# Performance work log

Hardware: AMD Instinct MI355X
Metric: run time of the kernel (lower is better)

Reference implementation:

```python
import jax, jax.numpy as jnp
import numpy as np

B, S, E, H = 4, 2048, 1024, 16
D = E // H  # head_dim = 64

def setup_inputs() -> dict:
    key = jax.random.key(0)
    ks = jax.random.split(key, 9)
    std = 1.0 / np.sqrt(E)
    return {
        "x":  jax.random.normal(ks[0], (B, S, E), jnp.float32),
        "Wq": jax.random.uniform(ks[1], (E, E), jnp.float32, -std, std),
        "bq": jax.random.uniform(ks[2], (E,),   jnp.float32, -std, std),
        "Wk": jax.random.uniform(ks[3], (E, E), jnp.float32, -std, std),
        "bk": jax.random.uniform(ks[4], (E,),   jnp.float32, -std, std),
        "Wv": jax.random.uniform(ks[5], (E, E), jnp.float32, -std, std),
        "bv": jax.random.uniform(ks[6], (E,),   jnp.float32, -std, std),
        "Wo": jax.random.uniform(ks[7], (E, E), jnp.float32, -std, std),
        "bo": jax.random.uniform(ks[8], (E,),   jnp.float32, -std, std),
    }

def reference(x, Wq, bq, Wk, bk, Wv, bv, Wo, bo):
    b, s, e = x.shape
    # QKV projections (weights stored as [in,out] == torch W.T applied as x @ W)
    q = (x @ Wq + bq).reshape(b, s, H, D).transpose(0, 2, 1, 3)  # [B,H,S,D]
    k = (x @ Wk + bk).reshape(b, s, H, D).transpose(0, 2, 1, 3)
    v = (x @ Wv + bv).reshape(b, s, H, D).transpose(0, 2, 1, 3)
    scores = jnp.einsum('bhqd,bhkd->bhqk', q, k) / jnp.sqrt(jnp.float32(D))
    causal = jnp.triu(jnp.ones((s, s), bool), k=1)  # True above diagonal
    scores = jnp.where(causal, -jnp.inf, scores)
    p = jax.nn.softmax(scores, axis=-1)  # dropout disabled (eval mode)
    out = jnp.einsum('bhqk,bhkd->bhqd', p, v)  # [B,H,S,D]
    out = out.transpose(0, 2, 1, 3).reshape(b, s, e)
    return out @ Wo + bo
```

## Files before the change

### kernel.cpp

```cpp
#include <hip/hip_runtime.h>
#include <math.h>

#define E_DIM 1024
#define B_DIM 4
#define S_DIM 2048
#define H_DIM 16
#define D_HEAD 64
#define M_DIM (B_DIM * S_DIM)
#define LOG2E 1.44269504f

typedef _Float16 half8 __attribute__((ext_vector_type(8)));
typedef _Float16 half4 __attribute__((ext_vector_type(4)));
typedef __fp16  fp16x2 __attribute__((ext_vector_type(2)));
typedef float floatx4 __attribute__((ext_vector_type(4)));
typedef unsigned uint2v __attribute__((ext_vector_type(2)));
#define MFMA_F16(a, b, c) __builtin_amdgcn_mfma_f32_16x16x32_f16(a, b, c, 0, 0, 0)

#if __has_builtin(__builtin_amdgcn_exp2f)
#define EXP2F(x) __builtin_amdgcn_exp2f(x)
#else
#define EXP2F(x) exp2f(x)
#endif

union H4 { fp16x2 h2[2]; half4 h4; };
union H8 { fp16x2 h2[4]; half8 h8; };

#define GLDS16(g, l)                                                          \
    __builtin_amdgcn_global_load_lds(                                         \
        (const __attribute__((address_space(1))) void*)(g),                   \
        (__attribute__((address_space(3))) void*)(l), 16, 0, 0)

__device__ const int QBAL[16] = {15,13,11,9, 0,2,4,6, 14,12,10,8, 1,3,5,7};

__global__ __launch_bounds__(256) void cvt_all(
    const float* __restrict__ X, _Float16* __restrict__ Xh,
    const float* __restrict__ W0, const float* __restrict__ W1,
    const float* __restrict__ W2, const float* __restrict__ W3,
    _Float16* __restrict__ T0, _Float16* __restrict__ T1,
    _Float16* __restrict__ T2, _Float16* __restrict__ T3)
{
    const int Lb = blockIdx.x;
    const int tid = threadIdx.x;
    if (Lb < 4096) {
        size_t i = ((size_t)Lb * 256 + tid) * 8;
        float4 a = *(const float4*)&X[i];
        float4 b = *(const float4*)&X[i + 4];
        half8 h = {(_Float16)a.x, (_Float16)a.y, (_Float16)a.z, (_Float16)a.w,
                   (_Float16)b.x, (_Float16)b.y, (_Float16)b.z, (_Float16)b.w};
        *(half8*)&Xh[i] = h;
        return;
    }
    const int L = Lb - 4096;
    const int z = L >> 8;
    const int rem = L & 255;
    const int k0 = (rem & 15) * 64, n0 = (rem >> 4) * 64;
    const float* W = (z == 0) ? W0 : (z == 1) ? W1 : (z == 2) ? W2 : W3;
    _Float16*   T  = (z == 0) ? T0 : (z == 1) ? T1 : (z == 2) ? T2 : T3;
    __shared__ float t[64][65];
#pragma unroll
    for (int it = 0; it < 4; it++) {
        int r = it * 16 + (tid >> 4);
        int c = (tid & 15) * 4;
        float4 v = *(const float4*)&W[(size_t)(k0 + r) * E_DIM + n0 + c];
        t[r][c] = v.x; t[r][c + 1] = v.y; t[r][c + 2] = v.z; t[r][c + 3] = v.w;
    }
    __syncthreads();
#pragma unroll
    for (int it = 0; it < 2; it++) {
        int n = it * 32 + (tid >> 3);
        int kk = (tid & 7) * 8;
        half8 h;
#pragma unroll
        for (int j = 0; j < 8; j++) h[j] = (_Float16)t[kk + j][n];
        *(half8*)&T[(size_t)(n0 + n) * E_DIM + k0 + kk] = h;
    }
}

#define STAGE128(t, s)                                                        \
    _Pragma("unroll") for (int i = 0; i < 4; i++) {                           \
        GLDS16(aS[i] + (t) * 64, As + (s) * 8192 + dOff[i]);                  \
        GLDS16(bS[i] + (t) * 64, Bs + (s) * 8192 + dOff[i]);                  \
    }

#define PH128_READ_A(mh)                                                      \
    _Pragma("unroll") for (int am = 0; am < 2; am++)                          \
        _Pragma("unroll") for (int kh = 0; kh < 2; kh++)                      \
            a_[am][kh] = *(const half8*)&As[sb +                              \
                (wr * 64 + ((mh) * 2 + am) * 16 + m16) * 64 +                 \
                (((kh * 4 + quad) ^ sw8) * 8)];

#define PH128_READ_B(nh)                                                      \
    _Pragma("unroll") for (int bn = 0; bn < 2; bn++)                          \
        _Pragma("unroll") for (int kh = 0; kh < 2; kh++)                      \
            b_[bn][kh] = *(const half8*)&Bs[sb +                              \
                (wc * 64 + ((nh) * 2 + bn) * 16 + m16) * 64 +                 \
                (((kh * 4 + quad) ^ sw8) * 8)];

#define PH128_MFMA(mh, nh)                                                    \
    __builtin_amdgcn_s_setprio(1);                                            \
    _Pragma("unroll") for (int am = 0; am < 2; am++)                          \
        _Pragma("unroll") for (int bn = 0; bn < 2; bn++)                      \
            acc[(mh) * 2 + am][(nh) * 2 + bn] =                               \
                MFMA_F16(a_[am][1], b_[bn][1],                                \
                    MFMA_F16(a_[am][0], b_[bn][0],                            \
                             acc[(mh) * 2 + am][(nh) * 2 + bn]));             \
    __builtin_amdgcn_s_setprio(0);

#define GEMM128_CORE(Aptr, Bptr)                                              \
    const int tid = threadIdx.x;                                              \
    const int wave = tid >> 6, lane = tid & 63;                               \
    const int m16 = lane & 15, quad = lane >> 4;                              \
    const int wr = wave >> 1, wc = wave & 1;                                  \
    const int m0 = blockIdx.x * 128, n0 = blockIdx.y * 128;                   \
    const int sw8 = m16 & 7;                                                  \
    __shared__ _Float16 As[2 * 8192];                                         \
    __shared__ _Float16 Bs[2 * 8192];                                         \
    floatx4 acc[4][4];                                                        \
    const floatx4 zf = {0.f, 0.f, 0.f, 0.f};                                  \
    _Pragma("unroll") for (int i = 0; i < 4; i++)                             \
        _Pragma("unroll") for (int j = 0; j < 4; j++) acc[i][j] = zf;         \
    const _Float16* aS[4];                                                    \
    const _Float16* bS[4];                                                    \
    int dOff[4];                                                              \
    _Pragma("unroll") for (int i = 0; i < 4; i++) {                           \
        int u = i * 256 + tid;                                                \
        int ru = u >> 3, cb = (u & 7) ^ (ru & 7);                             \
        aS[i] = (Aptr) + (size_t)(m0 + ru) * E_DIM + cb * 8;                  \
        bS[i] = (Bptr) + (size_t)(n0 + ru) * E_DIM + cb * 8;                  \
        dOff[i] = i * 2048 + wave * 512;                                      \
    }                                                                         \
    STAGE128(0, 0);                                                           \
    STAGE128(1, 1);                                                           \
    asm volatile("s_waitcnt vmcnt(8)" ::: "memory");                          \
    __builtin_amdgcn_s_barrier();                                             \
    half8 a_[2][2], b_[2][2];                                                 \
    for (int t = 0; t < 16; t++) {                                            \
        const int sb = (t & 1) * 8192;                                        \
        PH128_READ_A(0); PH128_READ_B(0); PH128_MFMA(0, 0);                   \
        PH128_READ_B(1); PH128_MFMA(0, 1);                                    \
        PH128_READ_A(1); PH128_MFMA(1, 1);                                    \
        PH128_READ_B(0); PH128_MFMA(1, 0);                                    \
        if (t + 1 < 16) {                                                     \
            asm volatile("s_waitcnt lgkmcnt(0)" ::: "memory");                \
            __builtin_amdgcn_s_barrier();                                     \
            if (t + 2 < 16) {                                                 \
                STAGE128(t + 2, t & 1);                                       \
                asm volatile("s_waitcnt vmcnt(8)" ::: "memory");              \
            } else {                                                          \
                asm volatile("s_waitcnt vmcnt(0)" ::: "memory");              \
            }                                                                 \
            __builtin_amdgcn_s_barrier();                                     \
        }                                                                     \
    }

__global__ __launch_bounds__(256) void qkv_mfma(
    const _Float16* __restrict__ Xh,
    const _Float16* __restrict__ Tq, const float* __restrict__ bq,
    const _Float16* __restrict__ Tk, const float* __restrict__ bk,
    const _Float16* __restrict__ Tv, const float* __restrict__ bv,
    _Float16* __restrict__ Qo, _Float16* __restrict__ Ko, _Float16* __restrict__ Vo)
{
    const int z = blockIdx.z;
    const _Float16* Wt   = (z == 0) ? Tq : (z == 1) ? Tk : Tv;
    const float*    bias = (z == 0) ? bq : (z == 1) ? bk : bv;

    GEMM128_CORE(Xh, Wt)

    if (z == 2) {
#pragma unroll
        for (int nt = 0; nt < 4; nt++) {
            int n = n0 + wc * 64 + nt * 16 + m16;
            int h = n >> 6, d = n & 63;
            int dt = d >> 4, ld = d & 15;
            float bias_v = bias[n];
#pragma unroll
            for (int mt = 0; mt < 4; mt++) {
                int m_b = m0 + wr * 64 + mt * 16 + quad * 4;
                int b = m_b >> 11, s = m_b & 2047;
                int bh = b * H_DIM + h;
                int c = s >> 6, kl = s & 63;
                int kh = kl >> 5, q8 = (kl >> 2) & 3, j0 = ((kl >> 4) & 1) * 4;
                size_t off = ((size_t)bh * 32 + c) * 4096
                           + (size_t)(((dt * 2 + kh) * 64 + q8 * 16 + ld) * 8 + j0);
                half4 hv;
#pragma unroll
                for (int r = 0; r < 4; r++) hv[r] = (_Float16)(acc[mt][nt][r] + bias_v);
                *(half4*)&Vo[off] = hv;
            }
        }
    } else {
        _Float16* Out = (z == 0) ? Qo : Ko;
        const float sc = (z == 0) ? 0.125f * LOG2E : 1.0f;
#pragma unroll
        for (int nt = 0; nt < 4; nt++) {
            int n = n0 + wc * 64 + nt * 16 + m16;
            int h = n >> 6, d = n & 63;
            int dh = d >> 5, qd = (d >> 3) & 3, j = d & 7;
            float bias_v = bias[n];
#pragma unroll
            for (int mt = 0; mt < 4; mt++) {
#pragma unroll
                for (int r = 0; r < 4; r++) {
                    int m = m0 + wr * 64 + mt * 16 + quad * 4 + r;
                    int b = m >> 11, s = m & 2047;
                    int bh = b * H_DIM + h;
                    size_t off;
                    if (z == 0) {
                        int qblk = s >> 7, qq = s & 127;
                        int sub = qq >> 4, lq = qq & 15;
                        off = ((size_t)bh * 16 + qblk) * 8192
                            + (size_t)(((sub * 2 + dh) * 64 + qd * 16 + lq) * 8 + j);
                    } else {
                        int c = s >> 6, kl = s & 63;
                        int kt = kl >> 4, lk = kl & 15;
                        off = ((size_t)bh * 32 + c) * 4096
                            + (size_t)(((kt * 2 + dh) * 64 + qd * 16 + lk) * 8 + j);
                    }
                    Out[off] = (_Float16)((acc[mt][nt][r] + bias_v) * sc);
                }
            }
        }
    }
}

__global__ __launch_bounds__(256) void out_mfma(
    const _Float16* __restrict__ Oh, const _Float16* __restrict__ To,
    const float* __restrict__ bias, float* __restrict__ Out)
{
    GEMM128_CORE(Oh, To)

#pragma unroll
    for (int nt = 0; nt < 4; nt++) {
        int n = n0 + wc * 64 + nt * 16 + m16;
        float bias_v = bias[n];
#pragma unroll
        for (int mt = 0; mt < 4; mt++) {
#pragma unroll
            for (int r = 0; r < 4; r++) {
                int m = m0 + wr * 64 + mt * 16 + quad * 4 + r;
                Out[(size_t)m * E_DIM + n] = acc[mt][nt][r] + bias_v;
            }
        }
    }
}

__global__ __launch_bounds__(256) void attn_mfma(
    const _Float16* __restrict__ Qb, const _Float16* __restrict__ Kb,
    const _Float16* __restrict__ Vb, _Float16* __restrict__ O)
{
    const int L = blockIdx.x;
    const int xcd = L & 7;
    const int u = L >> 3;
    const int cu = u & 31;
    const int rr = u >> 5;
    const int bh = xcd * 8 + (cu >> 2);
    const int qblk = QBAL[(cu & 3) + rr * 4];
    const int wave = threadIdx.x >> 6;
    const int lane = threadIdx.x & 63;
    const int m16 = lane & 15, quad = lane >> 4;

    const int qmin = qblk * 128 + wave * 32;
    const int c1w = ((qmin + 31) >> 6) + 1;

    const floatx4 zf  = {0.f, 0.f, 0.f, 0.f};
    const floatx4 cm4 = {-4.f, -4.f, -4.f, -4.f};
    half8 onev;
#pragma unroll
    for (int j = 0; j < 8; j++) onev[j] = (_Float16)1.0f;

    const _Float16* gQ = Qb + ((size_t)bh * 16 + qblk) * 8192
                            + wave * 2048 + lane * 8;
    half8 qf[2][2];
#pragma unroll
    for (int mt = 0; mt < 2; mt++)
#pragma unroll
        for (int dh = 0; dh < 2; dh++)
            qf[mt][dh] = *(const half8*)&gQ[(mt * 2 + dh) * 512];

    floatx4 acco[2][4];
    floatx4 lacc[2];
#pragma unroll
    for (int mt = 0; mt < 2; mt++) {
        lacc[mt] = zf;
#pragma unroll
        for (int dt = 0; dt < 4; dt++) acco[mt][dt] = zf;
    }

    const _Float16* gK = Kb + (size_t)bh * 131072 + lane * 8;
    const _Float16* gV = Vb + (size_t)bh * 131072 + lane * 8;

    half8 kf[4][2];
#pragma unroll
    for (int kt = 0; kt < 4; kt++)
#pragma unroll
        for (int dh = 0; dh < 2; dh++)
            kf[kt][dh] = *(const half8*)&gK[(kt * 2 + dh) * 512];
    gK += 4096;

    for (int c = 0; c < c1w; c++) {
        const int k0 = c * 64;

        half8 vf[4][2];
#pragma unroll
        for (int dt = 0; dt < 4; dt++)
#pragma unroll
            for (int kh = 0; kh < 2; kh++)
                vf[dt][kh] = *(const half8*)&gV[(dt * 2 + kh) * 512];
        gV += 4096;

        floatx4 sf[2][4];
        __builtin_amdgcn_s_setprio(1);
#pragma unroll
        for (int kt = 0; kt < 4; kt++)
#pragma unroll
            for (int mt = 0; mt < 2; mt++)
                sf[mt][kt] = MFMA_F16(kf[kt][1], qf[mt][1],
                               MFMA_F16(kf[kt][0], qf[mt][0], cm4));
        __builtin_amdgcn_s_setprio(0);

        if (c + 1 < c1w) {
#pragma unroll
            for (int kt = 0; kt < 4; kt++)
#pragma unroll
                for (int dh = 0; dh < 2; dh++)
                    kf[kt][dh] = *(const half8*)&gK[(kt * 2 + dh) * 512];
            gK += 4096;
        }

        const bool full = (k0 + 63 <= qmin);
#pragma unroll
        for (int mt = 0; mt < 2; mt++) {
            const int qg = qmin + mt * 16 + m16;
#pragma unroll
            for (int kt = 0; kt < 4; kt++)
#pragma unroll
                for (int r = 0; r < 4; r++) {
                    if (!full) {
                        int key = k0 + kt * 16 + quad * 4 + r;
                        if (key > qg) sf[mt][kt][r] = -INFINITY;
                    }
                }

            H8 u8[2];
#pragma unroll
            for (int kt = 0; kt < 4; kt++) {
                float e0 = EXP2F(sf[mt][kt][0]);
                float e1 = EXP2F(sf[mt][kt][1]);
                float e2 = EXP2F(sf[mt][kt][2]);
                float e3 = EXP2F(sf[mt][kt][3]);
                u8[kt >> 1].h2[(kt & 1) * 2]     = __builtin_amdgcn_cvt_pkrtz(e0, e1);
                u8[kt >> 1].h2[(kt & 1) * 2 + 1] = __builtin_amdgcn_cvt_pkrtz(e2, e3);
            }

            __builtin_amdgcn_s_setprio(1);
            lacc[mt] = MFMA_F16(onev, u8[1].h8,
                         MFMA_F16(onev, u8[0].h8, lacc[mt]));
#pragma unroll
            for (int dt = 0; dt < 4; dt++)
                acco[mt][dt] = MFMA_F16(vf[dt][1], u8[1].h8,
                                 MFMA_F16(vf[dt][0], u8[0].h8, acco[mt][dt]));
            __builtin_amdgcn_s_setprio(0);
        }
    }

    const int b_ = bh >> 4;
    const int h_ = bh & (H_DIM - 1);
#pragma unroll
    for (int mt = 0; mt < 2; mt++) {
        float inv = 1.f / lacc[mt][0];
        int q = qmin + mt * 16 + m16;
        _Float16* dst = O + (size_t)(b_ * S_DIM + q) * E_DIM + h_ * 64;
#pragma unroll
        for (int dt = 0; dt < 4; dt++) {
            H4 u4;
            u4.h2[0] = __builtin_amdgcn_cvt_pkrtz(acco[mt][dt][0] * inv, acco[mt][dt][1] * inv);
            u4.h2[1] = __builtin_amdgcn_cvt_pkrtz(acco[mt][dt][2] * inv, acco[mt][dt][3] * inv);
            *(half4*)&dst[dt * 16 + quad * 4] = u4.h4;
        }
    }
}

extern "C" void kernel_launch(void* const* d_in, const int* in_sizes, int n_in,
                              void* d_out, int out_size, void* d_ws, size_t ws_size,
                              hipStream_t stream) {
    const float* x  = (const float*)d_in[0];
    const float* Wq = (const float*)d_in[1];
    const float* bq = (const float*)d_in[2];
    const float* Wk = (const float*)d_in[3];
    const float* bk = (const float*)d_in[4];
    const float* Wv = (const float*)d_in[5];
    const float* bv = (const float*)d_in[6];
    const float* Wo = (const float*)d_in[7];
    const float* bo = (const float*)d_in[8];

    const size_t SZ = (size_t)M_DIM * E_DIM;
    const size_t WZ = (size_t)E_DIM * E_DIM;
    _Float16* Xh = (_Float16*)d_ws;
    _Float16* Tq = Xh + SZ;
    _Float16* Tk = Tq + WZ;
    _Float16* Tv = Tk + WZ;
    _Float16* To = Tv + WZ;
    _Float16* Qb = To + WZ;
    _Float16* Kb = Qb + SZ;
    _Float16* Vb = Kb + SZ;
    _Float16* Oh = Xh;

    cvt_all<<<dim3(4096 + 1024), 256, 0, stream>>>(
        x, Xh, Wq, Wk, Wv, Wo, Tq, Tk, Tv, To);

    qkv_mfma<<<dim3(M_DIM / 128, E_DIM / 128, 3), 256, 0, stream>>>(
        Xh, Tq, bq, Tk, bk, Tv, bv, Qb, Kb, Vb);

    attn_mfma<<<dim3(1024), 256, 0, stream>>>(Qb, Kb, Vb, Oh);

    out_mfma<<<dim3(M_DIM / 128, E_DIM / 128), 256, 0, stream>>>(
        Oh, To, bo, (float*)d_out);
}
```

Measured before the change: 258.2 us.

## Replace static attention tile mapping with per-wave atomic work queue

The attention kernel no longer uses a fixed block-to-tile mapping with a balancing table. Each wave now pulls 32-row query tiles from a global atomic counter, longest causal tiles first, so waves that finish early take more work. The counter is zeroed in the conversion kernel. This trades per-tile atomic traffic, and the loss of K/V locality between the waves of a block, for better dynamic load balance across causal tiles of uneven length. It also adds a launch bound hint of 4.

```diff
diff --git a/kernel.cpp b/kernel.cpp
--- a/kernel.cpp
+++ b/kernel.cpp
@@ -30,17 +30,17 @@
         (const __attribute__((address_space(1))) void*)(g),                   \
         (__attribute__((address_space(3))) void*)(l), 16, 0, 0)
 
-__device__ const int QBAL[16] = {15,13,11,9, 0,2,4,6, 14,12,10,8, 1,3,5,7};
-
 __global__ __launch_bounds__(256) void cvt_all(
     const float* __restrict__ X, _Float16* __restrict__ Xh,
     const float* __restrict__ W0, const float* __restrict__ W1,
     const float* __restrict__ W2, const float* __restrict__ W3,
     _Float16* __restrict__ T0, _Float16* __restrict__ T1,
-    _Float16* __restrict__ T2, _Float16* __restrict__ T3)
+    _Float16* __restrict__ T2, _Float16* __restrict__ T3,
+    unsigned* __restrict__ ctr)
 {
     const int Lb = blockIdx.x;
     const int tid = threadIdx.x;
+    if (Lb == 0 && tid == 0) *ctr = 0;
     if (Lb < 4096) {
         size_t i = ((size_t)Lb * 256 + tid) * 8;
         float4 a = *(const float4*)&X[i];
@@ -244,23 +244,13 @@
     }
 }
 
-__global__ __launch_bounds__(256) void attn_mfma(
+__global__ __launch_bounds__(256, 4) void attn_mfma(
     const _Float16* __restrict__ Qb, const _Float16* __restrict__ Kb,
-    const _Float16* __restrict__ Vb, _Float16* __restrict__ O)
+    const _Float16* __restrict__ Vb, _Float16* __restrict__ O,
+    unsigned* __restrict__ ctr)
 {
-    const int L = blockIdx.x;
-    const int xcd = L & 7;
-    const int u = L >> 3;
-    const int cu = u & 31;
-    const int rr = u >> 5;
-    const int bh = xcd * 8 + (cu >> 2);
-    const int qblk = QBAL[(cu & 3) + rr * 4];
-    const int wave = threadIdx.x >> 6;
     const int lane = threadIdx.x & 63;
     const int m16 = lane & 15, quad = lane >> 4;
-
-    const int qmin = qblk * 128 + wave * 32;
-    const int c1w = ((qmin + 31) >> 6) + 1;
 
     const floatx4 zf  = {0.f, 0.f, 0.f, 0.f};
     const floatx4 cm4 = {-4.f, -4.f, -4.f, -4.f};
@@ -268,114 +258,129 @@
 #pragma unroll
     for (int j = 0; j < 8; j++) onev[j] = (_Float16)1.0f;
 
-    const _Float16* gQ = Qb + ((size_t)bh * 16 + qblk) * 8192
-                            + wave * 2048 + lane * 8;
-    half8 qf[2][2];
-#pragma unroll
-    for (int mt = 0; mt < 2; mt++)
-#pragma unroll
-        for (int dh = 0; dh < 2; dh++)
-            qf[mt][dh] = *(const half8*)&gQ[(mt * 2 + dh) * 512];
-
-    floatx4 acco[2][4];
-    floatx4 lacc[2];
-#pragma unroll
-    for (int mt = 0; mt < 2; mt++) {
-        lacc[mt] = zf;
-#pragma unroll
-        for (int dt = 0; dt < 4; dt++) acco[mt][dt] = zf;
-    }
-
-    const _Float16* gK = Kb + (size_t)bh * 131072 + lane * 8;
-    const _Float16* gV = Vb + (size_t)bh * 131072 + lane * 8;
-
-    half8 kf[4][2];
-#pragma unroll
-    for (int kt = 0; kt < 4; kt++)
-#pragma unroll
-        for (int dh = 0; dh < 2; dh++)
-            kf[kt][dh] = *(const half8*)&gK[(kt * 2 + dh) * 512];
-    gK += 4096;
-
-    for (int c = 0; c < c1w; c++) {
-        const int k0 = c * 64;
-
-        half8 vf[4][2];
-#pragma unroll
-        for (int dt = 0; dt < 4; dt++)
-#pragma unroll
-            for (int kh = 0; kh < 2; kh++)
-                vf[dt][kh] = *(const half8*)&gV[(dt * 2 + kh) * 512];
-        gV += 4096;
-
-        floatx4 sf[2][4];
-        __builtin_amdgcn_s_setprio(1);
+    for (;;) {
+        unsigned tno = 0;
+        if (lane == 0) tno = atomicAdd(ctr, 1u);
+        tno = (unsigned)__builtin_amdgcn_readfirstlane((int)tno);
+        if (tno >= 4096u) break;
+
+        const int qblk = 15 - (int)(tno >> 8);
+        const int r8 = (int)(tno & 255u);
+        const int bh = r8 >> 2;
+        const int sl = r8 & 3;
+
+        const int qmin = qblk * 128 + sl * 32;
+        const int c1w = ((qmin + 31) >> 6) + 1;
+
+        const _Float16* gQ = Qb + ((size_t)bh * 16 + qblk) * 8192
+                                + sl * 2048 + lane * 8;
+        half8 qf[2][2];
+#pragma unroll
+        for (int mt = 0; mt < 2; mt++)
+#pragma unroll
+            for (int dh = 0; dh < 2; dh++)
+                qf[mt][dh] = *(const half8*)&gQ[(mt * 2 + dh) * 512];
+
+        floatx4 acco[2][4];
+        floatx4 lacc[2];
+#pragma unroll
+        for (int mt = 0; mt < 2; mt++) {
+            lacc[mt] = zf;
+#pragma unroll
+            for (int dt = 0; dt < 4; dt++) acco[mt][dt] = zf;
+        }
+
+        const _Float16* gK = Kb + (size_t)bh * 131072 + lane * 8;
+        const _Float16* gV = Vb + (size_t)bh * 131072 + lane * 8;
+
+        half8 kf[4][2];
 #pragma unroll
         for (int kt = 0; kt < 4; kt++)
 #pragma unroll
-            for (int mt = 0; mt < 2; mt++)
-                sf[mt][kt] = MFMA_F16(kf[kt][1], qf[mt][1],
-                               MFMA_F16(kf[kt][0], qf[mt][0], cm4));
-        __builtin_amdgcn_s_setprio(0);
-
-        if (c + 1 < c1w) {
+            for (int dh = 0; dh < 2; dh++)
+                kf[kt][dh] = *(const half8*)&gK[(kt * 2 + dh) * 512];
+        gK += 4096;
+
+        for (int c = 0; c < c1w; c++) {
+            const int k0 = c * 64;
+
+            half8 vf[4][2];
+#pragma unroll
+            for (int dt = 0; dt < 4; dt++)
+#pragma unroll
+                for (int kh = 0; kh < 2; kh++)
+                    vf[dt][kh] = *(const half8*)&gV[(dt * 2 + kh) * 512];
+            gV += 4096;
+
+            floatx4 sf[2][4];
+            __builtin_amdgcn_s_setprio(1);
 #pragma unroll
             for (int kt = 0; kt < 4; kt++)
 #pragma unroll
-                for (int dh = 0; dh < 2; dh++)
-                    kf[kt][dh] = *(const half8*)&gK[(kt * 2 + dh) * 512];
-            gK += 4096;
-        }
-
-        const bool full = (k0 + 63 <= qmin);
+                for (int mt = 0; mt < 2; mt++)
+                    sf[mt][kt] = MFMA_F16(kf[kt][1], qf[mt][1],
+                                   MFMA_F16(kf[kt][0], qf[mt][0], cm4));
+            __builtin_amdgcn_s_setprio(0);
+
+            if (c + 1 < c1w) {
+#pragma unroll
+                for (int kt = 0; kt < 4; kt++)
+#pragma unroll
+                    for (int dh = 0; dh < 2; dh++)
+                        kf[kt][dh] = *(const half8*)&gK[(kt * 2 + dh) * 512];
+                gK += 4096;
+            }
+
+            const bool full = (k0 + 63 <= qmin);
+#pragma unroll
+            for (int mt = 0; mt < 2; mt++) {
+                const int qg = qmin + mt * 16 + m16;
+#pragma unroll
+                for (int kt = 0; kt < 4; kt++)
+#pragma unroll
+                    for (int r = 0; r < 4; r++) {
+                        if (!full) {
+                            int key = k0 + kt * 16 + quad * 4 + r;
+                            if (key > qg) sf[mt][kt][r] = -INFINITY;
+                        }
+                    }
+
+                H8 u8[2];
+#pragma unroll
+                for (int kt = 0; kt < 4; kt++) {
+                    float e0 = EXP2F(sf[mt][kt][0]);
+                    float e1 = EXP2F(sf[mt][kt][1]);
+                    float e2 = EXP2F(sf[mt][kt][2]);
+                    float e3 = EXP2F(sf[mt][kt][3]);
+                    u8[kt >> 1].h2[(kt & 1) * 2]     = __builtin_amdgcn_cvt_pkrtz(e0, e1);
+                    u8[kt >> 1].h2[(kt & 1) * 2 + 1] = __builtin_amdgcn_cvt_pkrtz(e2, e3);
+                }
+
+                __builtin_amdgcn_s_setprio(1);
+                lacc[mt] = MFMA_F16(onev, u8[1].h8,
+                             MFMA_F16(onev, u8[0].h8, lacc[mt]));
+#pragma unroll
+                for (int dt = 0; dt < 4; dt++)
+                    acco[mt][dt] = MFMA_F16(vf[dt][1], u8[1].h8,
+                                     MFMA_F16(vf[dt][0], u8[0].h8, acco[mt][dt]));
+                __builtin_amdgcn_s_setprio(0);
+            }
+        }
+
+        const int b_ = bh >> 4;
+        const int h_ = bh & (H_DIM - 1);
 #pragma unroll
         for (int mt = 0; mt < 2; mt++) {
-            const int qg = qmin + mt * 16 + m16;
-#pragma unroll
-            for (int kt = 0; kt < 4; kt++)
-#pragma unroll
-                for (int r = 0; r < 4; r++) {
-                    if (!full) {
-                        int key = k0 + kt * 16 + quad * 4 + r;
-                        if (key > qg) sf[mt][kt][r] = -INFINITY;
-                    }
-                }
-
-            H8 u8[2];
-#pragma unroll
-            for (int kt = 0; kt < 4; kt++) {
-                float e0 = EXP2F(sf[mt][kt][0]);
-                float e1 = EXP2F(sf[mt][kt][1]);
-                float e2 = EXP2F(sf[mt][kt][2]);
-                float e3 = EXP2F(sf[mt][kt][3]);
-                u8[kt >> 1].h2[(kt & 1) * 2]     = __builtin_amdgcn_cvt_pkrtz(e0, e1);
-                u8[kt >> 1].h2[(kt & 1) * 2 + 1] = __builtin_amdgcn_cvt_pkrtz(e2, e3);
-            }
-
-            __builtin_amdgcn_s_setprio(1);
-            lacc[mt] = MFMA_F16(onev, u8[1].h8,
-                         MFMA_F16(onev, u8[0].h8, lacc[mt]));
-#pragma unroll
-            for (int dt = 0; dt < 4; dt++)
-                acco[mt][dt] = MFMA_F16(vf[dt][1], u8[1].h8,
-                                 MFMA_F16(vf[dt][0], u8[0].h8, acco[mt][dt]));
-            __builtin_amdgcn_s_setprio(0);
-        }
-    }
-
-    const int b_ = bh >> 4;
-    const int h_ = bh & (H_DIM - 1);
-#pragma unroll
-    for (int mt = 0; mt < 2; mt++) {
-        float inv = 1.f / lacc[mt][0];
-        int q = qmin + mt * 16 + m16;
-        _Float16* dst = O + (size_t)(b_ * S_DIM + q) * E_DIM + h_ * 64;
-#pragma unroll
-        for (int dt = 0; dt < 4; dt++) {
-            H4 u4;
-            u4.h2[0] = __builtin_amdgcn_cvt_pkrtz(acco[mt][dt][0] * inv, acco[mt][dt][1] * inv);
-            u4.h2[1] = __builtin_amdgcn_cvt_pkrtz(acco[mt][dt][2] * inv, acco[mt][dt][3] * inv);
-            *(half4*)&dst[dt * 16 + quad * 4] = u4.h4;
+            float inv = 1.f / lacc[mt][0];
+            int q = qmin + mt * 16 + m16;
+            _Float16* dst = O + (size_t)(b_ * S_DIM + q) * E_DIM + h_ * 64;
+#pragma unroll
+            for (int dt = 0; dt < 4; dt++) {
+                H4 u4;
+                u4.h2[0] = __builtin_amdgcn_cvt_pkrtz(acco[mt][dt][0] * inv, acco[mt][dt][1] * inv);
+                u4.h2[1] = __builtin_amdgcn_cvt_pkrtz(acco[mt][dt][2] * inv, acco[mt][dt][3] * inv);
+                *(half4*)&dst[dt * 16 + quad * 4] = u4.h4;
+            }
         }
     }
 }
@@ -403,15 +408,16 @@
     _Float16* Qb = To + WZ;
     _Float16* Kb = Qb + SZ;
     _Float16* Vb = Kb + SZ;
+    unsigned* Ctr = (unsigned*)(Vb + SZ);
     _Float16* Oh = Xh;
 
     cvt_all<<<dim3(4096 + 1024), 256, 0, stream>>>(
-        x, Xh, Wq, Wk, Wv, Wo, Tq, Tk, Tv, To);
+        x, Xh, Wq, Wk, Wv, Wo, Tq, Tk, Tv, To, Ctr);
 
     qkv_mfma<<<dim3(M_DIM / 128, E_DIM / 128, 3), 256, 0, stream>>>(
         Xh, Tq, bq, Tk, bk, Tv, bv, Qb, Kb, Vb);
 
-    attn_mfma<<<dim3(1024), 256, 0, stream>>>(Qb, Kb, Vb, Oh);
+    attn_mfma<<<dim3(1024), 256, 0, stream>>>(Qb, Kb, Vb, Oh, Ctr);
 
     out_mfma<<<dim3(M_DIM / 128, E_DIM / 128), 256, 0, stream>>>(
         Oh, To, bo, (float*)d_out);
```

New measurement: 632.6 us. 2.45x slower.
